# Kernel tuning notes

Measured on AMD Instinct MI355X. Metric: run time of the kernel, lower is better.

## Reference

```python
import jax, jax.numpy as jnp
import numpy as np


def setup_inputs() -> dict:
    key = jax.random.key(0)
    k1, k2 = jax.random.split(key)
    B1, B2, S0, K = 16, 16, 64, 64  # K = state_size
    e1 = jax.random.normal(k1, (B1, B2, 2, S0, K), dtype=jnp.float32)
    e2 = jax.random.normal(k2, (B1, B2, 2, K, K), dtype=jnp.float32)
    return {"e1": e1, "e2": e2}


def reference(e1, e2):
    # Faithful to CheckNodeTrellis.call (batch_dims=2):
    # res[b1,b2,u1,s0,s2] = logsumexp_{u2 in {0,1}, s1 in [K]}(
    #     e1[b1,b2,(u1+u2)%2,s0,s1] + e2[b1,b2,u2,s1,s2] )
    # The original builds meshgrid/tile gather_nd indices; here the index
    # arithmetic is expressed algebraically via a 2x2 parity table + broadcast.
    parity = (jnp.arange(2)[:, None] + jnp.arange(2)[None, :]) % 2  # [u1, u2]
    E1 = e1[:, :, parity, :, :]                    # [B1,B2,u1,u2,S0,K]
    # terms: [B1,B2,u1,u2,S0,s1,s2]
    terms = E1[..., None] + e2[:, :, None, :, None, :, :]
    # reduce over u2 (axis 3) and s1 (axis 5)
    return jax.scipy.special.logsumexp(terms, axis=(3, 5))
```

## Files before the change

### kernel.cpp

```cpp
#include <hip/hip_runtime.h>


__global__ __launch_bounds__(256) void trellis_lse_kernel(
    const float* __restrict__ e1,
    const float* __restrict__ e2,
    float* __restrict__ out)
{
    __shared__ float As[2048];
    __shared__ float Ad[2048];
    __shared__ float Bs[4096];
    __shared__ float Bd[4096];

    const int tid  = threadIdx.x;
    const int pair = blockIdx.x >> 1;
    const int h    = blockIdx.x & 1;
    const size_t base = (size_t)pair * 8192;

    const float4* __restrict__ e1v = (const float4*)(e1 + base);
    const float4* __restrict__ e2v = (const float4*)(e2 + base);
    float4* Asv = (float4*)As;
    float4* Adv = (float4*)Ad;
    float4* Bsv = (float4*)Bs;
    float4* Bdv = (float4*)Bd;

    const int h512 = h << 9;
    #pragma unroll
    for (int rr = 0; rr < 2; ++rr) {
        const int f = rr * 256 + tid;
        float4 a0 = e1v[h512 + f];
        float4 a1 = e1v[1024 + h512 + f];
        float4 s4, d4;
        float ea, eb;
        ea = __expf(a0.x); eb = __expf(a1.x); s4.x = ea + eb; d4.x = ea - eb;
        ea = __expf(a0.y); eb = __expf(a1.y); s4.y = ea + eb; d4.y = ea - eb;
        ea = __expf(a0.z); eb = __expf(a1.z); s4.z = ea + eb; d4.z = ea - eb;
        ea = __expf(a0.w); eb = __expf(a1.w); s4.w = ea + eb; d4.w = ea - eb;
        Asv[f] = s4; Adv[f] = d4;
    }
    #pragma unroll
    for (int rr = 0; rr < 4; ++rr) {
        const int f = rr * 256 + tid;
        float4 b0 = e2v[f];
        float4 b1 = e2v[1024 + f];
        float4 s4, d4;
        float ea, eb;
        ea = __expf(b0.x); eb = __expf(b1.x); s4.x = ea + eb; d4.x = ea - eb;
        ea = __expf(b0.y); eb = __expf(b1.y); s4.y = ea + eb; d4.y = ea - eb;
        ea = __expf(b0.z); eb = __expf(b1.z); s4.z = ea + eb; d4.z = ea - eb;
        ea = __expf(b0.w); eb = __expf(b1.w); s4.w = ea + eb; d4.w = ea - eb;
        Bsv[f] = s4; Bdv[f] = d4;
    }
    __syncthreads();

    const int w    = tid >> 6;
    const int lane = tid & 63;
    const int row0 = w << 3;

    float accU[8], accV[8];
    #pragma unroll
    for (int r = 0; r < 8; ++r) { accU[r] = 0.0f; accV[r] = 0.0f; }

    #pragma unroll 4
    for (int k4 = 0; k4 < 16; ++k4) {
        const int k = k4 << 2;
        const float bs0 = Bs[(k + 0) * 64 + lane];
        const float bs1 = Bs[(k + 1) * 64 + lane];
        const float bs2 = Bs[(k + 2) * 64 + lane];
        const float bs3 = Bs[(k + 3) * 64 + lane];
        const float bd0 = Bd[(k + 0) * 64 + lane];
        const float bd1 = Bd[(k + 1) * 64 + lane];
        const float bd2 = Bd[(k + 2) * 64 + lane];
        const float bd3 = Bd[(k + 3) * 64 + lane];
        #pragma unroll
        for (int r = 0; r < 8; ++r) {
            const float4 ap = *(const float4*)&As[(row0 + r) * 64 + k];
            const float4 ad = *(const float4*)&Ad[(row0 + r) * 64 + k];
            accU[r] = fmaf(ap.x, bs0, accU[r]);
            accU[r] = fmaf(ap.y, bs1, accU[r]);
            accU[r] = fmaf(ap.z, bs2, accU[r]);
            accU[r] = fmaf(ap.w, bs3, accU[r]);
            accV[r] = fmaf(ad.x, bd0, accV[r]);
            accV[r] = fmaf(ad.y, bd1, accV[r]);
            accV[r] = fmaf(ad.z, bd2, accV[r]);
            accV[r] = fmaf(ad.w, bd3, accV[r]);
        }
    }

    float* __restrict__ o0 = out + base + (size_t)((h << 5) + row0) * 64 + lane;
    float* __restrict__ o1 = o0 + 4096;
    #pragma unroll
    for (int r = 0; r < 8; ++r) {
        const float u = accU[r];
        const float v = accV[r];
        o0[r * 64] = __logf(0.5f * (u + v));
        o1[r * 64] = __logf(0.5f * (u - v));
    }
}

extern "C" void kernel_launch(void* const* d_in, const int* in_sizes, int n_in,
                              void* d_out, int out_size, void* d_ws, size_t ws_size,
                              hipStream_t stream)
{
    const float* e1 = (const float*)d_in[0];
    const float* e2 = (const float*)d_in[1];
    float* out = (float*)d_out;
    hipLaunchKernelGGL(trellis_lse_kernel, dim3(512), dim3(256), 0, stream,
                       e1, e2, out);
}
```

Baseline: 76.20 us.

## Compute exp-space trellis products with bf16 MFMA instead of FP32 FMAs

Replaces the scalar FP32 sum/difference matmul with bf16 MFMA 16x16x32 instructions. Exponentiated inputs are rounded to bf16, stored in padded LDS tiles, and the two parity products are accumulated directly with four MFMAs per tile instead of the sum/difference trick. Block ordering is also changed so both halves of a pair are spread across the grid. This cuts ALU work, but bf16 rounding of exp values lowers precision, and the unguarded exp/log still has the same overflow risk as before.

```diff
diff --git a/kernel.cpp b/kernel.cpp
--- a/kernel.cpp
+++ b/kernel.cpp
@@ -1,99 +1,120 @@
 #include <hip/hip_runtime.h>
 
 
-__global__ __launch_bounds__(256) void trellis_lse_kernel(
+typedef short short4v __attribute__((ext_vector_type(4)));
+typedef short short8v __attribute__((ext_vector_type(8)));
+typedef float float4v __attribute__((ext_vector_type(4)));
+
+#define LDA 72
+#define LDB 68
+
+__device__ __forceinline__ short expbf(float x) {
+    float f = __expf(x);
+    unsigned u = __builtin_bit_cast(unsigned, f);
+    u += 0x7fffu + ((u >> 16) & 1u);
+    return (short)(u >> 16);
+}
+
+__global__ __launch_bounds__(256) void trellis_mfma_kernel(
     const float* __restrict__ e1,
     const float* __restrict__ e2,
     float* __restrict__ out)
 {
-    __shared__ float As[2048];
-    __shared__ float Ad[2048];
-    __shared__ float Bs[4096];
-    __shared__ float Bd[4096];
+    __shared__ __align__(16) short A0s[32 * LDA];
+    __shared__ __align__(16) short A1s[32 * LDA];
+    __shared__ __align__(16) short B0s[64 * LDB];
+    __shared__ __align__(16) short B1s[64 * LDB];
 
     const int tid  = threadIdx.x;
-    const int pair = blockIdx.x >> 1;
-    const int h    = blockIdx.x & 1;
+    const int pair = blockIdx.x & 255;
+    const int h    = blockIdx.x >> 8;
     const size_t base = (size_t)pair * 8192;
 
     const float4* __restrict__ e1v = (const float4*)(e1 + base);
     const float4* __restrict__ e2v = (const float4*)(e2 + base);
-    float4* Asv = (float4*)As;
-    float4* Adv = (float4*)Ad;
-    float4* Bsv = (float4*)Bs;
-    float4* Bdv = (float4*)Bd;
 
-    const int h512 = h << 9;
     #pragma unroll
-    for (int rr = 0; rr < 2; ++rr) {
-        const int f = rr * 256 + tid;
-        float4 a0 = e1v[h512 + f];
-        float4 a1 = e1v[1024 + h512 + f];
-        float4 s4, d4;
-        float ea, eb;
-        ea = __expf(a0.x); eb = __expf(a1.x); s4.x = ea + eb; d4.x = ea - eb;
-        ea = __expf(a0.y); eb = __expf(a1.y); s4.y = ea + eb; d4.y = ea - eb;
-        ea = __expf(a0.z); eb = __expf(a1.z); s4.z = ea + eb; d4.z = ea - eb;
-        ea = __expf(a0.w); eb = __expf(a1.w); s4.w = ea + eb; d4.w = ea - eb;
-        Asv[f] = s4; Adv[f] = d4;
+    for (int it = 0; it < 2; ++it) {
+        const int f = it * 256 + tid;
+        const int r = f >> 4, c4 = f & 15;
+        const float4 a0 = e1v[h * 512 + f];
+        const float4 a1 = e1v[1024 + h * 512 + f];
+        short4v p0, p1;
+        p0.x = expbf(a0.x); p0.y = expbf(a0.y); p0.z = expbf(a0.z); p0.w = expbf(a0.w);
+        p1.x = expbf(a1.x); p1.y = expbf(a1.y); p1.z = expbf(a1.z); p1.w = expbf(a1.w);
+        *(short4v*)&A0s[r * LDA + c4 * 4] = p0;
+        *(short4v*)&A1s[r * LDA + c4 * 4] = p1;
     }
     #pragma unroll
-    for (int rr = 0; rr < 4; ++rr) {
-        const int f = rr * 256 + tid;
-        float4 b0 = e2v[f];
-        float4 b1 = e2v[1024 + f];
-        float4 s4, d4;
-        float ea, eb;
-        ea = __expf(b0.x); eb = __expf(b1.x); s4.x = ea + eb; d4.x = ea - eb;
-        ea = __expf(b0.y); eb = __expf(b1.y); s4.y = ea + eb; d4.y = ea - eb;
-        ea = __expf(b0.z); eb = __expf(b1.z); s4.z = ea + eb; d4.z = ea - eb;
-        ea = __expf(b0.w); eb = __expf(b1.w); s4.w = ea + eb; d4.w = ea - eb;
-        Bsv[f] = s4; Bdv[f] = d4;
+    for (int it = 0; it < 4; ++it) {
+        const int f = it * 256 + tid;
+        const int k = f >> 4, c4 = f & 15;
+        const float4 b0 = e2v[f];
+        const float4 b1 = e2v[1024 + f];
+        short4v p0, p1;
+        p0.x = expbf(b0.x); p0.y = expbf(b0.y); p0.z = expbf(b0.z); p0.w = expbf(b0.w);
+        p1.x = expbf(b1.x); p1.y = expbf(b1.y); p1.z = expbf(b1.z); p1.w = expbf(b1.w);
+        *(short4v*)&B0s[k * LDB + c4 * 4] = p0;
+        *(short4v*)&B1s[k * LDB + c4 * 4] = p1;
     }
     __syncthreads();
 
     const int w    = tid >> 6;
     const int lane = tid & 63;
-    const int row0 = w << 3;
+    const int ln   = lane & 15;
+    const int g    = lane >> 4;
+    const int r0   = (w >> 1) * 16;
+    const int c0   = (w & 1) * 32;
 
-    float accU[8], accV[8];
+    short8v a0f[2], a1f[2];
     #pragma unroll
-    for (int r = 0; r < 8; ++r) { accU[r] = 0.0f; accV[r] = 0.0f; }
+    for (int ks = 0; ks < 2; ++ks) {
+        const int off = (r0 + ln) * LDA + ks * 32 + g * 8;
+        a0f[ks] = *(const short8v*)&A0s[off];
+        a1f[ks] = *(const short8v*)&A1s[off];
+    }
 
-    #pragma unroll 4
-    for (int k4 = 0; k4 < 16; ++k4) {
-        const int k = k4 << 2;
-        const float bs0 = Bs[(k + 0) * 64 + lane];
-        const float bs1 = Bs[(k + 1) * 64 + lane];
-        const float bs2 = Bs[(k + 2) * 64 + lane];
-        const float bs3 = Bs[(k + 3) * 64 + lane];
-        const float bd0 = Bd[(k + 0) * 64 + lane];
-        const float bd1 = Bd[(k + 1) * 64 + lane];
-        const float bd2 = Bd[(k + 2) * 64 + lane];
-        const float bd3 = Bd[(k + 3) * 64 + lane];
+    short8v b0f[2][2], b1f[2][2];
+    #pragma unroll
+    for (int ct = 0; ct < 2; ++ct) {
         #pragma unroll
-        for (int r = 0; r < 8; ++r) {
-            const float4 ap = *(const float4*)&As[(row0 + r) * 64 + k];
-            const float4 ad = *(const float4*)&Ad[(row0 + r) * 64 + k];
-            accU[r] = fmaf(ap.x, bs0, accU[r]);
-            accU[r] = fmaf(ap.y, bs1, accU[r]);
-            accU[r] = fmaf(ap.z, bs2, accU[r]);
-            accU[r] = fmaf(ap.w, bs3, accU[r]);
-            accV[r] = fmaf(ad.x, bd0, accV[r]);
-            accV[r] = fmaf(ad.y, bd1, accV[r]);
-            accV[r] = fmaf(ad.z, bd2, accV[r]);
-            accV[r] = fmaf(ad.w, bd3, accV[r]);
+        for (int ks = 0; ks < 2; ++ks) {
+            const int col = c0 + ct * 16 + ln;
+            const int kb  = ks * 32 + g * 8;
+            short8v t0, t1;
+            #pragma unroll
+            for (int i = 0; i < 8; ++i) {
+                t0[i] = B0s[(kb + i) * LDB + col];
+                t1[i] = B1s[(kb + i) * LDB + col];
+            }
+            b0f[ct][ks] = t0;
+            b1f[ct][ks] = t1;
         }
     }
 
-    float* __restrict__ o0 = out + base + (size_t)((h << 5) + row0) * 64 + lane;
-    float* __restrict__ o1 = o0 + 4096;
+    float4v acc0[2] = {{0.f,0.f,0.f,0.f}, {0.f,0.f,0.f,0.f}};
+    float4v acc1[2] = {{0.f,0.f,0.f,0.f}, {0.f,0.f,0.f,0.f}};
     #pragma unroll
-    for (int r = 0; r < 8; ++r) {
-        const float u = accU[r];
-        const float v = accV[r];
-        o0[r * 64] = __logf(0.5f * (u + v));
-        o1[r * 64] = __logf(0.5f * (u - v));
+    for (int ct = 0; ct < 2; ++ct) {
+        #pragma unroll
+        for (int ks = 0; ks < 2; ++ks) {
+            acc0[ct] = __builtin_amdgcn_mfma_f32_16x16x32_bf16(a0f[ks], b0f[ct][ks], acc0[ct], 0, 0, 0);
+            acc0[ct] = __builtin_amdgcn_mfma_f32_16x16x32_bf16(a1f[ks], b1f[ct][ks], acc0[ct], 0, 0, 0);
+            acc1[ct] = __builtin_amdgcn_mfma_f32_16x16x32_bf16(a1f[ks], b0f[ct][ks], acc1[ct], 0, 0, 0);
+            acc1[ct] = __builtin_amdgcn_mfma_f32_16x16x32_bf16(a0f[ks], b1f[ct][ks], acc1[ct], 0, 0, 0);
+        }
+    }
+
+    const int srow0 = 32 * h + r0 + g * 4;
+    #pragma unroll
+    for (int ct = 0; ct < 2; ++ct) {
+        const int col = c0 + ct * 16 + ln;
+        #pragma unroll
+        for (int j = 0; j < 4; ++j) {
+            const size_t o = base + (size_t)(srow0 + j) * 64 + col;
+            out[o]        = __logf(acc0[ct][j]);
+            out[o + 4096] = __logf(acc1[ct][j]);
+        }
     }
 }
 
@@ -104,6 +125,6 @@
     const float* e1 = (const float*)d_in[0];
     const float* e2 = (const float*)d_in[1];
     float* out = (float*)d_out;
-    hipLaunchKernelGGL(trellis_lse_kernel, dim3(512), dim3(256), 0, stream,
+    hipLaunchKernelGGL(trellis_mfma_kernel, dim3(512), dim3(256), 0, stream,
                        e1, e2, out);
 }
```

New measurement: 69.39 us. 1.1x faster.
